# Kernel tuning notes

Measured on AMD Instinct MI355X. Metric: run time of the kernel, lower is better.

Reference implementation:

```python
import jax, jax.numpy as jnp
import numpy as np

N_NODES = 100000
N_EDGES = 3200000
D = 256
L = 3
BN_EPS = 1e-5


def setup_inputs() -> dict:
    key = jax.random.key(0)
    ks = jax.random.split(key, 6)
    scale = 1.0 / np.sqrt(D)
    x = jax.random.normal(ks[0], (N_NODES, D), dtype=jnp.float32)
    W = jax.random.normal(ks[1], (L, D, D), dtype=jnp.float32) * scale
    b = jnp.zeros((L, D), dtype=jnp.float32)
    Wl = jax.random.normal(ks[2], (L, D, D), dtype=jnp.float32) * scale
    bl = jnp.zeros((L, D), dtype=jnp.float32)
    gamma = jnp.ones((L, D), dtype=jnp.float32)
    beta = jnp.zeros((L, D), dtype=jnp.float32)
    src = jax.random.randint(ks[3], (N_EDGES,), 0, N_NODES, dtype=jnp.int32)
    dst = jax.random.randint(ks[4], (N_EDGES,), 0, N_NODES, dtype=jnp.int32)
    return {"x": x, "W": W, "b": b, "Wl": Wl, "bl": bl,
            "gamma": gamma, "beta": beta, "src": src, "dst": dst}


def _gcn_head(x, W, b, Wl, bl, gamma, beta, src, dst):
    n = x.shape[0]
    ones = jnp.ones((src.shape[0],), dtype=x.dtype)
    # degrees (clamped to 1, as DGL GraphConv does)
    deg_out = jnp.maximum(jax.ops.segment_sum(ones, src, num_segments=n), 1.0)
    deg_in = jnp.maximum(jax.ops.segment_sum(ones, dst, num_segments=n), 1.0)
    inv_sqrt_out = (deg_out ** -0.5)[:, None]  # [N,1]
    inv_sqrt_in = (deg_in ** -0.5)[:, None]

    h = x
    for l in range(W.shape[0]):
        # GraphConv, norm='both': D_in^{-1/2} A D_out^{-1/2} h W + b
        hs = h * inv_sqrt_out
        agg = jax.ops.segment_sum(hs[src], dst, num_segments=n)  # [N,D]
        agg = agg * inv_sqrt_in
        out = agg @ W[l] + b[l]
        # residual + optional linear on the layer input
        out = out + h + (h @ Wl[l] + bl[l])
        # BatchNorm1d over nodes (training-style batch stats, biased var)
        mean = jnp.mean(out, axis=0)
        var = jnp.var(out, axis=0)
        out = gamma[l] * (out - mean) * jax.lax.rsqrt(var + BN_EPS) + beta[l]
        # ReLU (Dropout treated as identity / eval mode)
        h = jax.nn.relu(out)
    return h


def reference(x, W, b, Wl, bl, gamma, beta, src, dst):
    return _gcn_head(x, W, b, Wl, bl, gamma, beta, src, dst)
```

## Files before the change

### kernel.cpp

```cpp
#include <hip/hip_runtime.h>

#define D 256
#define BN_EPS 1e-5f

typedef __attribute__((ext_vector_type(8))) short short8;
typedef __attribute__((ext_vector_type(4))) float f32x4;
typedef __attribute__((ext_vector_type(2))) float f32x2;

__device__ __forceinline__ float b2f(ushort u) {
    union { unsigned u; float f; } c; c.u = ((unsigned)u) << 16; return c.f;
}
__device__ __forceinline__ ushort f2b(float f) {
    union { float f; unsigned u; } c; c.f = f;
    return (ushort)((c.u + 0x7fffu + ((c.u >> 16) & 1u)) >> 16);
}

typedef __attribute__((address_space(1))) const void gv_t;
typedef __attribute__((address_space(3))) void lv_t;
__device__ __forceinline__ void gld16(const void* g, void* l) {
    __builtin_amdgcn_global_load_lds((gv_t*)g, (lv_t*)l, 16, 0, 0);
}

__device__ __forceinline__ uint2 pk_fp8x8(const float* r) {
    unsigned w0 = 0, w1 = 0;
    w0 = __builtin_amdgcn_cvt_pk_fp8_f32(r[0], r[1], w0, false);
    w0 = __builtin_amdgcn_cvt_pk_fp8_f32(r[2], r[3], w0, true);
    w1 = __builtin_amdgcn_cvt_pk_fp8_f32(r[4], r[5], w1, false);
    w1 = __builtin_amdgcn_cvt_pk_fp8_f32(r[6], r[7], w1, true);
    return make_uint2(w0, w1);
}


#define HB 64

__global__ __launch_bounds__(256) void hist_kernel(const int* __restrict__ src,
                                                   const int* __restrict__ dst,
                                                   unsigned* __restrict__ P, int E) {
    __shared__ unsigned lhist[16384];
    int combo = blockIdx.y;
    const int* arr = (combo >> 2) ? dst : src;
    unsigned base = (unsigned)(combo & 3) << 15;
    for (int j = threadIdx.x; j < 16384; j += 256) lhist[j] = 0;
    __syncthreads();
    int i0 = (blockIdx.x * 256 + threadIdx.x) * 4;
    int stride = HB * 256 * 4;
    for (int i = i0; i < E; i += stride) {
        if (i + 3 < E) {
            int4 v = *(const int4*)(arr + i);
            unsigned r0 = (unsigned)v.x - base;
            unsigned r1 = (unsigned)v.y - base;
            unsigned r2 = (unsigned)v.z - base;
            unsigned r3 = (unsigned)v.w - base;
            if (r0 < 32768u) atomicAdd(&lhist[r0 >> 1], 1u << ((r0 & 1) << 4));
            if (r1 < 32768u) atomicAdd(&lhist[r1 >> 1], 1u << ((r1 & 1) << 4));
            if (r2 < 32768u) atomicAdd(&lhist[r2 >> 1], 1u << ((r2 & 1) << 4));
            if (r3 < 32768u) atomicAdd(&lhist[r3 >> 1], 1u << ((r3 & 1) << 4));
        } else {
            for (int j = i; j < E; j++) {
                unsigned r = (unsigned)arr[j] - base;
                if (r < 32768u) atomicAdd(&lhist[r >> 1], 1u << ((r & 1) << 4));
            }
        }
    }
    __syncthreads();
    unsigned* dstp = P + ((size_t)(combo * HB + blockIdx.x) << 14);
    for (int j = threadIdx.x; j < 16384; j += 256) dstp[j] = lhist[j];
}

__global__ void histreduce_kernel(const unsigned* __restrict__ P,
                                  int* __restrict__ cntO, int* __restrict__ cntI, int N) {
    int g = blockIdx.x * 256 + threadIdx.x;
    int array = g >> 16;
    int p = g & 65535;
    int range = p >> 14;
    int j = p & 16383;
    const unsigned* Pp = P + ((size_t)((array * 4 + range) * HB) << 14) + j;
    unsigned s = 0;
#pragma unroll 8
    for (int b = 0; b < HB; b++) s += Pp[(size_t)b << 14];
    int bin = (range << 15) + 2 * j;
    int* cnt = array ? cntI : cntO;
    if (bin < N)     cnt[bin]     = (int)(s & 0xFFFFu);
    if (bin + 1 < N) cnt[bin + 1] = (int)(s >> 16);
}

__global__ void invsqrt_kernel(const int* __restrict__ cntO, const int* __restrict__ cntI,
                               float* __restrict__ invO, float* __restrict__ invOI,
                               float* __restrict__ sqrtO, int N) {
    int i = blockIdx.x * blockDim.x + threadIdx.x;
    if (i < N) {
        float dO = (float)max(cntO[i], 1);
        float io = rsqrtf(dO);
        invO[i] = io;
        sqrtO[i] = sqrtf(dO);
        invOI[i] = io * rsqrtf((float)max(cntI[i], 1));
    }
}

__global__ void scan1_kernel(const int* __restrict__ cnt, int* __restrict__ off,
                             int* __restrict__ bsum, int n) {
    __shared__ int s[256];
    int t = threadIdx.x;
    int i0 = blockIdx.x * 1024 + t * 4;
    int v0 = (i0 < n) ? ((cnt[i0] + 7) & ~7) : 0;
    int v1 = (i0 + 1 < n) ? ((cnt[i0 + 1] + 7) & ~7) : 0;
    int v2 = (i0 + 2 < n) ? ((cnt[i0 + 2] + 7) & ~7) : 0;
    int v3 = (i0 + 3 < n) ? ((cnt[i0 + 3] + 7) & ~7) : 0;
    int tsum = v0 + v1 + v2 + v3;
    s[t] = tsum;
    __syncthreads();
    for (int d = 1; d < 256; d <<= 1) {
        int x = (t >= d) ? s[t - d] : 0;
        __syncthreads();
        s[t] += x;
        __syncthreads();
    }
    int excl = s[t] - tsum;
    if (i0 < n)     off[i0]     = excl;
    if (i0 + 1 < n) off[i0 + 1] = excl + v0;
    if (i0 + 2 < n) off[i0 + 2] = excl + v0 + v1;
    if (i0 + 3 < n) off[i0 + 3] = excl + v0 + v1 + v2;
    if (t == 255) bsum[blockIdx.x] = s[255];
}

__global__ void scan2_kernel(int* __restrict__ bsum, int nb) {
    __shared__ int s[256];
    int t = threadIdx.x;
    int v = (t < nb) ? bsum[t] : 0;
    s[t] = v;
    __syncthreads();
    for (int d = 1; d < 256; d <<= 1) {
        int x = (t >= d) ? s[t - d] : 0;
        __syncthreads();
        s[t] += x;
        __syncthreads();
    }
    if (t < nb) bsum[t] = s[t] - v;
    if (t == nb - 1) bsum[1023] = s[t];
}

__global__ void scan3_kernel(int* __restrict__ off, const int* __restrict__ bsum,
                             int* __restrict__ bucketCur, int n) {
    int i = blockIdx.x * blockDim.x + threadIdx.x;
    if (i < n) {
        int v = off[i] + bsum[i >> 10];
        off[i] = v;
        if ((i & 255) == 0) bucketCur[i >> 8] = v;
    } else if (i == n) {
        off[n] = bsum[1023];
    }
}


#define NBKMAX 512

__global__ __launch_bounds__(256) void partA_kernel(const int* __restrict__ src,
                                                    const int* __restrict__ dst,
                                                    int* __restrict__ bucketCur,
                                                    unsigned* __restrict__ pairs,
                                                    int E, int NBK) {
    __shared__ int cnt[NBKMAX];
    __shared__ int base_s[NBKMAX];
    for (int j = threadIdx.x; j < NBK; j += 256) cnt[j] = 0;
    __syncthreads();
    for (int i = blockIdx.x * 256 + threadIdx.x; i < E; i += gridDim.x * 256)
        atomicAdd(&cnt[((unsigned)dst[i]) >> 8], 1);
    __syncthreads();
    for (int j = threadIdx.x; j < NBK; j += 256) {
        base_s[j] = atomicAdd(&bucketCur[j], cnt[j]);
        cnt[j] = 0;
    }
    __syncthreads();
    for (int i = blockIdx.x * 256 + threadIdx.x; i < E; i += gridDim.x * 256) {
        unsigned d = (unsigned)dst[i];
        unsigned b = d >> 8;
        int pos = base_s[b] + atomicAdd(&cnt[b], 1);
        pairs[pos] = ((unsigned)src[i] << 8) | (d & 255u);
    }
}

#define BCAP 14336

__global__ __launch_bounds__(256) void partB_kernel(const unsigned* __restrict__ pairs,
                                                    const int* __restrict__ off,
                                                    const int* __restrict__ bucketCur,
                                                    int* __restrict__ srcS, int N) {
    __shared__ int curL[256];
    __shared__ int stage[BCAP];
    int b = blockIdx.x;
    int n0 = b << 8;
    int n1 = min(n0 + 256, N);
    int base = off[n0];
    int len = off[n1] - base;
    if (len > BCAP) len = BCAP;
    for (int j = threadIdx.x; j < len; j += 256) stage[j] = N;
    int nn = n1 - n0;
    for (int i = threadIdx.x; i < nn; i += 256) curL[i] = off[n0 + i] - base;
    __syncthreads();
    int cntB = bucketCur[b] - base;
    for (int j = threadIdx.x; j < cntB; j += 256) {
        unsigned p = pairs[base + j];
        int pos = atomicAdd(&curL[p & 255u], 1);
        if (pos < BCAP) stage[pos] = (int)(p >> 8);
    }
    __syncthreads();
    for (int j4 = threadIdx.x; j4 * 4 < len; j4 += 256)
        *(int4*)(srcS + base + j4 * 4) = *(const int4*)(stage + j4 * 4);
}

__global__ void init_pad_kernel(ushort* __restrict__ X, unsigned* __restrict__ X8,
                                int N, long strideH) {
    int t = threadIdx.x;
    X[(size_t)N * D + t] = 0;
    if (t < 64) X8[(t >> 5) * strideH + (size_t)N * 32 + (t & 31)] = 0;
}


__global__ void prep_w_kernel(const float* __restrict__ W, const float* __restrict__ Wl,
                              const float* __restrict__ b, const float* __restrict__ bl,
                              ushort* __restrict__ Wt, float* __restrict__ bcat, int L) {
    int idx = blockIdx.x * blockDim.x + threadIdx.x;
    int k = idx & 511;
    int n = (idx >> 9) & 255;
    int l = idx >> 17;
    if (l >= L) return;
    float v;
    if (k < 256) {
        v = W[(size_t)l * 65536 + k * 256 + n];
    } else {
        v = Wl[(size_t)l * 65536 + (k - 256) * 256 + n];
        if (k - 256 == n) v += 1.0f;
    }
    Wt[idx] = f2b(v);
    if (k == 0) bcat[l * 256 + n] = b[l * 256 + n] + bl[l * 256 + n];
}

__global__ void x2b_kernel(const float* __restrict__ x, const float* __restrict__ invO,
                           ushort* __restrict__ hs, unsigned* __restrict__ hs8,
                           long strideH, long n8) {
    long i8 = (long)blockIdx.x * blockDim.x + threadIdx.x;
    if (i8 >= n8) return;
    long row = i8 >> 5;
    float sc = invO[row];
    float4 a = ((const float4*)x)[i8 * 2];
    float4 b = ((const float4*)x)[i8 * 2 + 1];
    float r[8] = { a.x * sc, a.y * sc, a.z * sc, a.w * sc,
                   b.x * sc, b.y * sc, b.z * sc, b.w * sc };
    ushort v[8];
#pragma unroll
    for (int j = 0; j < 8; j++) v[j] = f2b(r[j]);
    *(short8*)(hs + i8 * 8) = *(short8*)v;
    long H = (i8 >> 4) & 1;
    *(uint2*)(hs8 + H * strideH + row * 32 + (i8 & 15) * 2) = pk_fp8x8(r);
}


__global__ void aggregate_kernel(const unsigned* __restrict__ hs8h,
                                 const float* __restrict__ invOI,
                                 const int* __restrict__ off, const int* __restrict__ srcS,
                                 ushort* __restrict__ aggsh, int N) {
    int tid = threadIdx.x;
    int wid = tid >> 6, lane = tid & 63;
    int l32 = lane & 31;
    int node = blockIdx.x * 8 + wid * 2 + (lane >> 5);
    if (blockIdx.x * 8 + wid * 2 >= N) return;
    bool valid = node < N;
    int e0 = valid ? off[node] : 0;
    int e1 = valid ? off[node + 1] : 0;
    f32x2 A01 = {0.f, 0.f}, A23 = {0.f, 0.f};
    for (int e = e0; e < e1; e += 8) {
        int4 c0 = *(const int4*)(srcS + e);
        int4 c1 = *(const int4*)(srcS + e + 4);
        unsigned g0 = hs8h[(size_t)c0.x * 32 + l32];
        unsigned g1 = hs8h[(size_t)c0.y * 32 + l32];
        unsigned g2 = hs8h[(size_t)c0.z * 32 + l32];
        unsigned g3 = hs8h[(size_t)c0.w * 32 + l32];
        unsigned g4 = hs8h[(size_t)c1.x * 32 + l32];
        unsigned g5 = hs8h[(size_t)c1.y * 32 + l32];
        unsigned g6 = hs8h[(size_t)c1.z * 32 + l32];
        unsigned g7 = hs8h[(size_t)c1.w * 32 + l32];
#pragma unroll
        for (int q = 0; q < 8; q++) {
            unsigned g = (q == 0) ? g0 : (q == 1) ? g1 : (q == 2) ? g2 : (q == 3) ? g3
                       : (q == 4) ? g4 : (q == 5) ? g5 : (q == 6) ? g6 : g7;
            A01 += __builtin_amdgcn_cvt_pk_f32_fp8(g, false);
            A23 += __builtin_amdgcn_cvt_pk_f32_fp8(g, true);
        }
    }
    if (valid) {
        float wi = invOI[node];
        ushort4 o;
        o.x = f2b(A01[0] * wi); o.y = f2b(A01[1] * wi);
        o.z = f2b(A23[0] * wi); o.w = f2b(A23[1] * wi);
        *(ushort4*)(aggsh + (size_t)node * D + l32 * 4) = o;
    }
}


__global__ __launch_bounds__(256) void gemm_kernel(
        const ushort* __restrict__ aggs, const ushort* __restrict__ hs,
        const ushort* __restrict__ Wt,  const float* __restrict__ bcat,
        const float* __restrict__ sqrtO,
        ushort* __restrict__ tmp, float* __restrict__ bnsum, float* __restrict__ bnsq,
        int M) {
    __shared__ short As[2][128 * 32];
    __shared__ short Bs[2][128 * 32];

    int bid = blockIdx.x;
    int bm = (bid & 7) + (bid >> 4) * 8;
    int bn0 = ((bid >> 3) & 1) * 128;
    if (bm * 128 >= M) return;
    int bm0 = bm * 128;

    int tid = threadIdx.x;
    int wid = tid >> 6, lane = tid & 63;
    int wr = wid >> 1, wc = wid & 1;
    int lrow = lane & 15, lkh = lane >> 4;
    int srow = lane >> 2;
    int sseg = (lane & 3) ^ ((srow >> 1) & 3);

    const ushort* gbBase = Wt + (size_t)(bn0 + wid * 32 + srow) * 512 + sseg * 8;

    f32x4 acc[4][4] = {};

#define STAGE(buf, k0s)                                                                    \
    {                                                                                      \
        int kk_ = (k0s) & 255;                                                             \
        const ushort* Ah_ = ((k0s) < 256) ? aggs : hs;                                     \
        const ushort* ga_ = Ah_ + (size_t)(bm0 + wid * 32 + srow) * 256 + kk_ + sseg * 8;  \
        gld16(ga_,            &As[buf][(wid * 32) * 32]);                                  \
        gld16(ga_ + 16 * 256, &As[buf][(wid * 32 + 16) * 32]);                             \
        gld16(gbBase + (k0s),            &Bs[buf][(wid * 32) * 32]);                       \
        gld16(gbBase + (k0s) + 16 * 512, &Bs[buf][(wid * 32 + 16) * 32]);                  \
    }

    STAGE(0, 0);

#pragma unroll
    for (int k0 = 0; k0 < 512; k0 += 32) {
        int cur = (k0 >> 5) & 1;
        __syncthreads();
        if (k0 + 32 < 512) STAGE(cur ^ 1, k0 + 32);

        short8 a[4], bfr[4];
#pragma unroll
        for (int m = 0; m < 4; m++) {
            int ra = wr * 64 + m * 16 + lrow;
            a[m] = *(short8*)&As[cur][ra * 32 + (lkh ^ ((ra >> 1) & 3)) * 8];
        }
#pragma unroll
        for (int n = 0; n < 4; n++) {
            int rb = wc * 64 + n * 16 + lrow;
            bfr[n] = *(short8*)&Bs[cur][rb * 32 + (lkh ^ ((rb >> 1) & 3)) * 8];
        }
#pragma unroll
        for (int m = 0; m < 4; m++)
#pragma unroll
            for (int n = 0; n < 4; n++)
                acc[m][n] = __builtin_amdgcn_mfma_f32_16x16x32_bf16(a[m], bfr[n], acc[m][n], 0, 0, 0);
    }
#undef STAGE

#pragma unroll
    for (int n = 0; n < 4; n++) {
        int col = bn0 + wc * 64 + n * 16 + lrow;
        float bc = bcat[col];
        float s_part = 0.f, q_part = 0.f;
#pragma unroll
        for (int m = 0; m < 4; m++) {
            int rbase = bm0 + wr * 64 + m * 16 + lkh * 4;
#pragma unroll
            for (int i = 0; i < 4; i++) {
                int row = rbase + i;
                if (row < M) {
                    float v = acc[m][n][i] * sqrtO[row] + bc;
                    tmp[(size_t)row * D + col] = f2b(v);
                    s_part += v;
                    q_part += v * v;
                }
            }
        }
        s_part += __shfl_xor(s_part, 16);
        s_part += __shfl_xor(s_part, 32);
        q_part += __shfl_xor(q_part, 16);
        q_part += __shfl_xor(q_part, 32);
        if (lkh == 0) {
            atomicAdd(&bnsum[col], s_part);
            atomicAdd(&bnsq[col], q_part);
        }
    }
}


__global__ void bnfin_kernel(float* __restrict__ bnsum, float* __restrict__ bnsq,
                             const float* __restrict__ gamma, const float* __restrict__ beta,
                             float2* __restrict__ bnab, float invM) {
    int c = threadIdx.x;
    float mean = bnsum[c] * invM;
    float var = bnsq[c] * invM - mean * mean;
    float a = gamma[c] * rsqrtf(var + BN_EPS);
    bnab[c] = make_float2(a, beta[c] - a * mean);
    bnsum[c] = 0.f;
    bnsq[c] = 0.f;
}

__global__ void bnrelu_kernel(const ushort* __restrict__ tmp, const float2* __restrict__ bnab,
                              const float* __restrict__ invO, ushort* __restrict__ Xout,
                              unsigned* __restrict__ X8out, long strideH,
                              float* __restrict__ out, int M, int last) {
    long i8 = (long)blockIdx.x * blockDim.x + threadIdx.x;
    if (i8 >= (long)M * 32) return;
    long row = i8 >> 5;
    int c0 = ((int)(i8 & 31)) * 8;
    short8 v = *(const short8*)(tmp + row * D + c0);
    float r[8];
#pragma unroll
    for (int j = 0; j < 8; j++) {
        float2 ab = bnab[c0 + j];
        float x = b2f((ushort)v[j]);
        r[j] = fmaxf(ab.x * x + ab.y, 0.f);
    }
    if (last) {
        float4 f0 = make_float4(r[0], r[1], r[2], r[3]);
        float4 f1 = make_float4(r[4], r[5], r[6], r[7]);
        ((float4*)(out + row * D + c0))[0] = f0;
        ((float4*)(out + row * D + c0))[1] = f1;
    } else {
        float sc = invO[row];
        ushort w[8];
#pragma unroll
        for (int j = 0; j < 8; j++) { r[j] *= sc; w[j] = f2b(r[j]); }
        *(short8*)(Xout + row * D + c0) = *(short8*)w;
        long H = (i8 >> 4) & 1;
        *(uint2*)(X8out + H * strideH + row * 32 + (i8 & 15) * 2) = pk_fp8x8(r);
    }
}


extern "C" void kernel_launch(void* const* d_in, const int* in_sizes, int n_in,
                              void* d_out, int out_size, void* d_ws, size_t ws_size,
                              hipStream_t stream) {
    const float* x     = (const float*)d_in[0];
    const float* W     = (const float*)d_in[1];
    const float* b     = (const float*)d_in[2];
    const float* Wl    = (const float*)d_in[3];
    const float* bl    = (const float*)d_in[4];
    const float* gamma = (const float*)d_in[5];
    const float* beta  = (const float*)d_in[6];
    const int*   src   = (const int*)d_in[7];
    const int*   dst   = (const int*)d_in[8];

    const int N = in_sizes[0] / D;
    const int E = in_sizes[7];
    const int L = in_sizes[1] / (D * D);
    const int M_pad = (N + 1 + 127) & ~127;
    const int E_pad = E + 7 * N + 64;
    const int NBK = (N + 255) >> 8;
    const long strideH = (long)M_pad * 32;
    float* out = (float*)d_out;

    char* p = (char*)d_ws;
    auto alloc = [&](size_t bytes) -> char* {
        char* r = p;
        p += (bytes + 255) & ~(size_t)255;
        return r;
    };
    int*      cur   = (int*)alloc((size_t)NBKMAX * 4);
    int*      cntO  = (int*)alloc((size_t)N * 4);
    int*      cntI  = (int*)alloc((size_t)N * 4);
    float*    invO  = (float*)alloc((size_t)(N + 1) * 4);
    float*    invOI = (float*)alloc((size_t)(N + 1) * 4);
    float*    sqrtO = (float*)alloc((size_t)(N + 1) * 4);
    int*      off_  = (int*)alloc((size_t)(N + 1) * 4);
    int*      bsum  = (int*)alloc(1024 * 4);
    int*      srcS  = (int*)alloc((size_t)E_pad * 4);
    ushort*   Wt    = (ushort*)alloc((size_t)L * 256 * 512 * 2);
    float*    bcat  = (float*)alloc((size_t)L * 256 * 4);
    ushort*   X     = (ushort*)alloc((size_t)M_pad * D * 2);
    unsigned* X8    = (unsigned*)alloc((size_t)2 * strideH * 4);
    ushort*   aggs  = (ushort*)alloc((size_t)M_pad * D * 2);
    ushort*   tmp   = (ushort*)alloc((size_t)M_pad * D * 2);
    float*    bnsum = (float*)alloc((size_t)2 * D * 4);
    float*    bnsq  = bnsum + D;
    float2*   bnab  = (float2*)alloc((size_t)D * 8);

    unsigned* P     = (unsigned*)aggs;
    unsigned* pairs = (unsigned*)aggs;

    {
        dim3 hg(HB, 8);
        hist_kernel<<<hg, 256, 0, stream>>>(src, dst, P, E);
        histreduce_kernel<<<512, 256, 0, stream>>>(P, cntO, cntI, N);
    }
    invsqrt_kernel<<<(N + 255) / 256, 256, 0, stream>>>(cntO, cntI, invO, invOI, sqrtO, N);
    int NB = (N + 1023) / 1024;
    scan1_kernel<<<NB, 256, 0, stream>>>(cntI, off_, bsum, N);
    scan2_kernel<<<1, 256, 0, stream>>>(bsum, NB);
    scan3_kernel<<<(N + 256) / 256, 256, 0, stream>>>(off_, bsum, cur, N);
    partA_kernel<<<512, 256, 0, stream>>>(src, dst, cur, pairs, E, NBK);
    partB_kernel<<<NBK, 256, 0, stream>>>(pairs, off_, cur, srcS, N);
    init_pad_kernel<<<1, 256, 0, stream>>>(X, X8, N, strideH);

    prep_w_kernel<<<(L * 256 * 512 + 255) / 256, 256, 0, stream>>>(W, Wl, b, bl, Wt, bcat, L);
    x2b_kernel<<<(int)(((long)N * 32 + 255) / 256), 256, 0, stream>>>(
        x, invO, X, X8, strideH, (long)N * 32);
    hipMemsetAsync(bnsum, 0, 2 * D * sizeof(float), stream);

    const int MB = (N + 127) / 128;
    const int gemm_grid = ((MB + 7) >> 3) * 16;
    const int agg_grid = (N + 7) / 8;
    const float invM = 1.0f / (float)N;
    for (int l = 0; l < L; l++) {
        int last = (l == L - 1);

        aggregate_kernel<<<agg_grid, 256, 0, stream>>>(X8, invOI, off_, srcS, aggs, N);
        aggregate_kernel<<<agg_grid, 256, 0, stream>>>(X8 + strideH, invOI, off_, srcS,
                                                       aggs + 128, N);

        gemm_kernel<<<gemm_grid, 256, 0, stream>>>(aggs, X, Wt + (size_t)l * 256 * 512,
                                                   bcat + l * 256, sqrtO, tmp, bnsum, bnsq, N);

        bnfin_kernel<<<1, 256, 0, stream>>>(bnsum, bnsq, gamma + l * D, beta + l * D, bnab, invM);
        bnrelu_kernel<<<(int)(((long)N * 32 + 255) / 256), 256, 0, stream>>>(
            tmp, bnab, invO, X, X8, strideH, out, N, last);
    }
}
```

Before: 815.2 us.

## Widen GEMM tile to full 256 columns and stage output through LDS

The GEMM now uses 512-thread blocks that each compute a 128x256 tile covering all output columns. Each A tile is therefore loaded once rather than twice across two column blocks. The epilogue writes bf16 results into shared memory and then stores coalesced 16-byte rows to global memory, replacing scattered 2-byte stores. The cost is more LDS per block, extra barriers in the epilogue, and half as many blocks, which may lower occupancy.

```diff
diff --git a/kernel.cpp b/kernel.cpp
--- a/kernel.cpp
+++ b/kernel.cpp
@@ -297,29 +297,26 @@
 }
 
 
-__global__ __launch_bounds__(256) void gemm_kernel(
+#define ASOFF(buf) ((buf) * 4096)
+#define BSOFF(buf) (8192 + (buf) * 8192)
+
+__global__ __launch_bounds__(512) void gemm_kernel(
         const ushort* __restrict__ aggs, const ushort* __restrict__ hs,
         const ushort* __restrict__ Wt,  const float* __restrict__ bcat,
         const float* __restrict__ sqrtO,
         ushort* __restrict__ tmp, float* __restrict__ bnsum, float* __restrict__ bnsq,
         int M) {
-    __shared__ short As[2][128 * 32];
-    __shared__ short Bs[2][128 * 32];
-
-    int bid = blockIdx.x;
-    int bm = (bid & 7) + (bid >> 4) * 8;
-    int bn0 = ((bid >> 3) & 1) * 128;
-    if (bm * 128 >= M) return;
-    int bm0 = bm * 128;
+    __shared__ short SH[24576];
+
+    int bm0 = blockIdx.x * 128;
+    if (bm0 >= M) return;
 
     int tid = threadIdx.x;
     int wid = tid >> 6, lane = tid & 63;
-    int wr = wid >> 1, wc = wid & 1;
+    int wr = wid >> 2, wc = wid & 3;
     int lrow = lane & 15, lkh = lane >> 4;
     int srow = lane >> 2;
     int sseg = (lane & 3) ^ ((srow >> 1) & 3);
-
-    const ushort* gbBase = Wt + (size_t)(bn0 + wid * 32 + srow) * 512 + sseg * 8;
 
     f32x4 acc[4][4] = {};
 
@@ -327,11 +324,11 @@
     {                                                                                      \
         int kk_ = (k0s) & 255;                                                             \
         const ushort* Ah_ = ((k0s) < 256) ? aggs : hs;                                     \
-        const ushort* ga_ = Ah_ + (size_t)(bm0 + wid * 32 + srow) * 256 + kk_ + sseg * 8;  \
-        gld16(ga_,            &As[buf][(wid * 32) * 32]);                                  \
-        gld16(ga_ + 16 * 256, &As[buf][(wid * 32 + 16) * 32]);                             \
-        gld16(gbBase + (k0s),            &Bs[buf][(wid * 32) * 32]);                       \
-        gld16(gbBase + (k0s) + 16 * 512, &Bs[buf][(wid * 32 + 16) * 32]);                  \
+        gld16(Ah_ + (size_t)(bm0 + wid * 16 + srow) * 256 + kk_ + sseg * 8,                \
+              SH + ASOFF(buf) + (wid * 16) * 32);                                          \
+        const ushort* gb_ = Wt + (size_t)(wid * 32 + srow) * 512 + (k0s) + sseg * 8;       \
+        gld16(gb_,            SH + BSOFF(buf) + (wid * 32) * 32);                          \
+        gld16(gb_ + 16 * 512, SH + BSOFF(buf) + (wid * 32 + 16) * 32);                     \
     }
 
     STAGE(0, 0);
@@ -346,12 +343,12 @@
 #pragma unroll
         for (int m = 0; m < 4; m++) {
             int ra = wr * 64 + m * 16 + lrow;
-            a[m] = *(short8*)&As[cur][ra * 32 + (lkh ^ ((ra >> 1) & 3)) * 8];
+            a[m] = *(short8*)&SH[ASOFF(cur) + ra * 32 + (lkh ^ ((ra >> 1) & 3)) * 8];
         }
 #pragma unroll
         for (int n = 0; n < 4; n++) {
             int rb = wc * 64 + n * 16 + lrow;
-            bfr[n] = *(short8*)&Bs[cur][rb * 32 + (lkh ^ ((rb >> 1) & 3)) * 8];
+            bfr[n] = *(short8*)&SH[BSOFF(cur) + rb * 32 + (lkh ^ ((rb >> 1) & 3)) * 8];
         }
 #pragma unroll
         for (int m = 0; m < 4; m++)
@@ -361,9 +358,10 @@
     }
 #undef STAGE
 
+    ushort outv[4][4][4];
 #pragma unroll
     for (int n = 0; n < 4; n++) {
-        int col = bn0 + wc * 64 + n * 16 + lrow;
+        int col = wc * 64 + n * 16 + lrow;
         float bc = bcat[col];
         float s_part = 0.f, q_part = 0.f;
 #pragma unroll
@@ -372,12 +370,9 @@
 #pragma unroll
             for (int i = 0; i < 4; i++) {
                 int row = rbase + i;
-                if (row < M) {
-                    float v = acc[m][n][i] * sqrtO[row] + bc;
-                    tmp[(size_t)row * D + col] = f2b(v);
-                    s_part += v;
-                    q_part += v * v;
-                }
+                float v = (row < M) ? (acc[m][n][i] * sqrtO[row] + bc) : 0.f;
+                outv[m][n][i] = f2b(v);
+                if (row < M) { s_part += v; q_part += v * v; }
             }
         }
         s_part += __shfl_xor(s_part, 16);
@@ -387,6 +382,29 @@
         if (lkh == 0) {
             atomicAdd(&bnsum[col], s_part);
             atomicAdd(&bnsq[col], q_part);
+        }
+    }
+
+    for (int half = 0; half < 2; half++) {
+        __syncthreads();
+        if (wr == half) {
+#pragma unroll
+            for (int m = 0; m < 4; m++)
+#pragma unroll
+                for (int n = 0; n < 4; n++)
+#pragma unroll
+                    for (int i = 0; i < 4; i++)
+                        SH[(m * 16 + lkh * 4 + i) * 256 + wc * 64 + n * 16 + lrow] =
+                            (short)outv[m][n][i];
+        }
+        __syncthreads();
+#pragma unroll
+        for (int p = 0; p < 4; p++) {
+            int rl = (tid >> 5) + p * 16;
+            int row = bm0 + half * 64 + rl;
+            if (row < M)
+                *(short8*)(tmp + (size_t)row * 256 + (tid & 31) * 8) =
+                    *(short8*)&SH[rl * 256 + (tid & 31) * 8];
         }
     }
 }
@@ -507,7 +525,6 @@
     hipMemsetAsync(bnsum, 0, 2 * D * sizeof(float), stream);
 
     const int MB = (N + 127) / 128;
-    const int gemm_grid = ((MB + 7) >> 3) * 16;
     const int agg_grid = (N + 7) / 8;
     const float invM = 1.0f / (float)N;
     for (int l = 0; l < L; l++) {
@@ -517,8 +534,8 @@
         aggregate_kernel<<<agg_grid, 256, 0, stream>>>(X8 + strideH, invOI, off_, srcS,
                                                        aggs + 128, N);
 
-        gemm_kernel<<<gemm_grid, 256, 0, stream>>>(aggs, X, Wt + (size_t)l * 256 * 512,
-                                                   bcat + l * 256, sqrtO, tmp, bnsum, bnsq, N);
+        gemm_kernel<<<MB, 512, 0, stream>>>(aggs, X, Wt + (size_t)l * 256 * 512,
+                                            bcat + l * 256, sqrtO, tmp, bnsum, bnsq, N);
 
         bnfin_kernel<<<1, 256, 0, stream>>>(bnsum, bnsq, gamma + l * D, beta + l * D, bnab, invM);
         bnrelu_kernel<<<(int)(((long)N * 32 + 255) / 256), 256, 0, stream>>>(
```

New measurement: 764.5 us. 1.07x faster.
